# Performance work log

Measured on AMD Instinct MI355X. Metric: run time of the kernel, lower is better.

Reference implementation:

```python
import jax, jax.numpy as jnp
import numpy as np

B, T, D, H, FC, A = 256, 128, 512, 1024, 1024, 32
LOG_STD_MIN, LOG_STD_MAX = -20.0, 2.0
EPS = 1e-5


def setup_inputs() -> dict:
    key = jax.random.key(0)
    ks = jax.random.split(key, 16)
    def w(k, shape, fan_in):
        return jax.random.normal(k, shape, jnp.float32) / np.float32(np.sqrt(fan_in))
    return {
        "observations": jax.random.normal(ks[0], (B, T, D), jnp.float32),
        "hidden_state": jax.random.normal(ks[1], (B, H), jnp.float32),
        "episode_starts": jax.random.randint(ks[2], (B, T), 0, 2, jnp.int32),
        "ln_gamma": jnp.ones((D,), jnp.float32),
        "ln_beta": jnp.zeros((D,), jnp.float32),
        "W_fc": w(ks[3], (FC, D), D), "b_fc": jnp.zeros((FC,), jnp.float32),
        "W_ih": w(ks[4], (3 * H, FC), FC), "b_ih": jnp.zeros((3 * H,), jnp.float32),
        "W_hh": w(ks[5], (3 * H, H), H), "b_hh": jnp.zeros((3 * H,), jnp.float32),
        "W_out": w(ks[6], (H, H), H), "b_out": jnp.zeros((H,), jnp.float32),
        "W_mean": w(ks[7], (A, H), H) * 0.01, "b_mean": jnp.zeros((A,), jnp.float32),
        "W_ls": w(ks[8], (A, H), H) * 0.01, "b_ls": jnp.zeros((A,), jnp.float32),
    }


def reference(observations, hidden_state, episode_starts, ln_gamma, ln_beta,
              W_fc, b_fc, W_ih, b_ih, W_hh, b_hh, W_out, b_out,
              W_mean, b_mean, W_ls, b_ls):
    # LayerNorm over last dim (eps=1e-5, like nn.LayerNorm)
    mu = jnp.mean(observations, axis=-1, keepdims=True)
    var = jnp.mean(jnp.square(observations - mu), axis=-1, keepdims=True)
    x = (observations - mu) * jax.lax.rsqrt(var + EPS) * ln_gamma + ln_beta
    # fc_in + ReLU, then precompute GRU input-gate projections for all steps
    x = jax.nn.relu(jnp.einsum('btd,fd->btf', x, W_fc) + b_fc)          # (B,T,FC)
    xg = jnp.einsum('btf,gf->btg', x, W_ih) + b_ih                      # (B,T,3H)
    xg_t = jnp.swapaxes(xg, 0, 1)                                       # (T,B,3H)
    starts_t = jnp.swapaxes(episode_starts, 0, 1).astype(jnp.float32)   # (T,B)

    def step(h, inp):
        xg_s, st = inp
        h = h * (1.0 - st)[:, None]
        gh = h @ W_hh.T + b_hh                                           # (B,3H)
        xr, xz, xn = xg_s[:, :H], xg_s[:, H:2 * H], xg_s[:, 2 * H:]
        hr, hz, hn = gh[:, :H], gh[:, H:2 * H], gh[:, 2 * H:]
        r = jax.nn.sigmoid(xr + hr)
        z = jax.nn.sigmoid(xz + hz)
        n = jnp.tanh(xn + r * hn)
        h_new = (1.0 - z) * n + z * h
        out = jax.nn.relu(h_new @ W_out.T + b_out)
        return h_new, out

    h_final, outs = jax.lax.scan(step, hidden_state, (xg_t, starts_t))
    feats = jnp.swapaxes(outs, 0, 1)                                     # (B,T,H)
    means = jnp.einsum('bth,ah->bta', feats, W_mean) + b_mean
    log_std = jnp.clip(jnp.einsum('bth,ah->bta', feats, W_ls) + b_ls,
                       LOG_STD_MIN, LOG_STD_MAX)
    return means, log_std, h_final
```

## Files before the change

kernel.cpp:

```cpp
#include <hip/hip_runtime.h>
#include <hip/hip_bf16.h>

#define B_ 256
#define T_ 128
#define D_ 512
#define H_ 1024
#define FC_ 1024
#define A_ 32
#define NWG_ 256

typedef short bf16x8 __attribute__((ext_vector_type(8)));
typedef float f32x4 __attribute__((ext_vector_type(4)));

__device__ __forceinline__ float bf2f(unsigned short u) {
  return __uint_as_float(((unsigned)u) << 16);
}
__device__ __forceinline__ unsigned short f2bf(float x) {
  unsigned u = __float_as_uint(x);
  u = u + 0x7fffu + ((u >> 16) & 1u);
  return (unsigned short)(u >> 16);
}
__device__ __forceinline__ void unpack8(uint4 v, float* f) {
  f[0] = bf2f(v.x & 0xffff); f[1] = bf2f(v.x >> 16);
  f[2] = bf2f(v.y & 0xffff); f[3] = bf2f(v.y >> 16);
  f[4] = bf2f(v.z & 0xffff); f[5] = bf2f(v.z >> 16);
  f[6] = bf2f(v.w & 0xffff); f[7] = bf2f(v.w >> 16);
}
__device__ __forceinline__ uint4 pack8(const float* f) {
  uint4 v;
  v.x = (unsigned)f2bf(f[0]) | ((unsigned)f2bf(f[1]) << 16);
  v.y = (unsigned)f2bf(f[2]) | ((unsigned)f2bf(f[3]) << 16);
  v.z = (unsigned)f2bf(f[4]) | ((unsigned)f2bf(f[5]) << 16);
  v.w = (unsigned)f2bf(f[6]) | ((unsigned)f2bf(f[7]) << 16);
  return v;
}

__global__ __launch_bounds__(256) void detect_kernel(
    const unsigned short* __restrict__ obs, int* __restrict__ flag)
{
  __shared__ int cnt;
  if (threadIdx.x == 0) cnt = 0;
  __syncthreads();
  int c = 0;
  for (int i = threadIdx.x; i < 8192; i += 256) {
    unsigned e = (obs[i] >> 7) & 0xffu;
    if (e >= 0x86u) c++;
  }
  atomicAdd(&cnt, c);
  __syncthreads();
  if (threadIdx.x == 0) *flag = (cnt >= 64) ? 1 : 0;
}

struct CanonArgs {
  const void* src[14];
  unsigned short* dst[14];
  int ofs[15];
};
__global__ __launch_bounds__(256) void canon_kernel(CanonArgs a,
                                                    const int* __restrict__ flag)
{
  const int fl = *flag;
  const int i0 = (blockIdx.x * 256 + threadIdx.x) * 8;
  int t = 0;
  while (t < 14 && i0 >= a.ofs[t + 1]) t++;
  if (t >= 14) return;
  const int local = i0 - a.ofs[t];
  unsigned short* d = a.dst[t] + local;
  if (fl) {
    const float* s = (const float*)a.src[t] + local;
    #pragma unroll
    for (int e = 0; e < 8; e++) d[e] = f2bf(s[e]);
  } else {
    const unsigned short* s = (const unsigned short*)a.src[t] + local;
    #pragma unroll
    for (int e = 0; e < 8; e++) d[e] = s[e];
  }
}

__global__ __launch_bounds__(256) void ln_kernel(
    const void* __restrict__ obs,
    const unsigned short* __restrict__ gamma_,
    const unsigned short* __restrict__ beta_,
    unsigned short* __restrict__ xn, int t0, int tcShift,
    const int* __restrict__ flag)
{
  const int fl = *flag;
  const int lane = threadIdx.x & 63;
  const int rloc = blockIdx.x * 4 + (threadIdx.x >> 6);
  const int b  = rloc >> tcShift;
  const int tl = rloc & ((1 << tcShift) - 1);
  const int grow = b * T_ + t0 + tl;
  float f[8];
  if (fl) {
    const float* of = (const float*)obs + (size_t)grow * D_ + lane * 8;
    const float4 v0 = *(const float4*)of;
    const float4 v1 = *(const float4*)(of + 4);
    f[0] = v0.x; f[1] = v0.y; f[2] = v0.z; f[3] = v0.w;
    f[4] = v1.x; f[5] = v1.y; f[6] = v1.z; f[7] = v1.w;
  } else {
    uint4 v = *(const uint4*)((const unsigned short*)obs + (size_t)grow * D_ + lane * 8);
    unpack8(v, f);
  }
  float s = 0.f, ss = 0.f;
  #pragma unroll
  for (int i = 0; i < 8; i++) { s += f[i]; ss += f[i] * f[i]; }
  #pragma unroll
  for (int off = 32; off > 0; off >>= 1) {
    s  += __shfl_xor(s,  off, 64);
    ss += __shfl_xor(ss, off, 64);
  }
  const float mu  = s * (1.0f / D_);
  const float var = ss * (1.0f / D_) - mu * mu;
  const float inv = rsqrtf(var + 1e-5f);
  float g[8], b8[8];
  unpack8(*(const uint4*)(gamma_ + lane * 8), g);
  unpack8(*(const uint4*)(beta_  + lane * 8), b8);
  float o[8];
  #pragma unroll
  for (int i = 0; i < 8; i++) o[i] = (f[i] - mu) * inv * g[i] + b8[i];
  *(uint4*)(xn + (size_t)rloc * D_ + lane * 8) = pack8(o);
}

__global__ __launch_bounds__(256) void gemm_tn(
    const unsigned short* __restrict__ A, const unsigned short* __restrict__ Bm,
    const unsigned short* __restrict__ bias, unsigned short* __restrict__ C,
    int M, int N, int K, int relu)
{
  __shared__ short As[128][40];
  __shared__ short Bs[128][40];
  const int tid  = threadIdx.x;
  const int wave = tid >> 6, lane = tid & 63;
  const int quad = lane >> 4, l15 = lane & 15;
  const int m0 = blockIdx.y * 128, n0 = blockIdx.x * 128;
  const int wm = (wave >> 1) * 64, wn = (wave & 1) * 64;
  const int lrow = tid >> 2, lk = (tid & 3) * 8;
  f32x4 acc[4][4] = {};
  const size_t a0 = (size_t)(m0 + lrow) * K + lk;
  const size_t a1 = (size_t)(m0 + lrow + 64) * K + lk;
  const size_t b0 = (size_t)(n0 + lrow) * K + lk;
  const size_t b1 = (size_t)(n0 + lrow + 64) * K + lk;
  for (int k0 = 0; k0 < K; k0 += 32) {
    __syncthreads();
    *(uint4*)&As[lrow][lk]      = *(const uint4*)(A  + a0 + k0);
    *(uint4*)&As[lrow + 64][lk] = *(const uint4*)(A  + a1 + k0);
    *(uint4*)&Bs[lrow][lk]      = *(const uint4*)(Bm + b0 + k0);
    *(uint4*)&Bs[lrow + 64][lk] = *(const uint4*)(Bm + b1 + k0);
    __syncthreads();
    bf16x8 af[4], bfv[4];
    #pragma unroll
    for (int i = 0; i < 4; i++) af[i]  = *(const bf16x8*)&As[wm + i * 16 + l15][quad * 8];
    #pragma unroll
    for (int j = 0; j < 4; j++) bfv[j] = *(const bf16x8*)&Bs[wn + j * 16 + l15][quad * 8];
    #pragma unroll
    for (int i = 0; i < 4; i++)
      #pragma unroll
      for (int j = 0; j < 4; j++)
        acc[i][j] = __builtin_amdgcn_mfma_f32_16x16x32_bf16(af[i], bfv[j], acc[i][j], 0, 0, 0);
  }
  #pragma unroll
  for (int j = 0; j < 4; j++) {
    const int col = n0 + wn + j * 16 + l15;
    const float bj = bias ? bf2f(bias[col]) : 0.0f;
    #pragma unroll
    for (int i = 0; i < 4; i++) {
      const int row = m0 + wm + i * 16 + quad * 4;
      #pragma unroll
      for (int r = 0; r < 4; r++) {
        float v = acc[i][j][r] + bj;
        if (relu) v = fmaxf(v, 0.0f);
        C[(size_t)(row + r) * N + col] = f2bf(v);
      }
    }
  }
}

__global__ __launch_bounds__(256, 1) void gru_scan(
    const unsigned short* __restrict__ xg,
    const int* __restrict__ starts,
    const unsigned short* __restrict__ Whh,
    const unsigned short* __restrict__ bhh,
    float* __restrict__ hf,
    unsigned long long* __restrict__ hb0,
    unsigned long long* __restrict__ hb1,
    unsigned short* __restrict__ hall,
    int t0, int Tc,
    int* __restrict__ flags)
{
  __shared__ short Ws[3 * 16 * 1032];
  __shared__ short Hs[64 * 136];
  __shared__ unsigned sbits[64][4];
  const int tid  = threadIdx.x;
  const int wg   = blockIdx.x;
  const int jb   = wg & 63, bb = wg >> 6;
  const int j0   = jb * 16, b0 = bb * 64;
  const int wave = tid >> 6, lane = tid & 63;
  const int quad = lane >> 4, l15 = lane & 15;

  for (int c = tid; c < 48 * 128; c += 256) {
    const int row = c >> 7;
    const int kc  = (c & 127) * 8;
    const int g = row >> 4, jj = row & 15;
    *(uint4*)&Ws[row * 1032 + kc] =
        *(const uint4*)(Whh + (size_t)(g * H_ + j0 + jj) * H_ + kc);
  }
  for (int c = tid; c < 64 * 4; c += 256) {
    const int row = c >> 2, w = c & 3;
    unsigned m = 0;
    #pragma unroll
    for (int bi = 0; bi < 32; bi++)
      m |= (starts[(b0 + row) * T_ + w * 32 + bi] ? 1u : 0u) << bi;
    sbits[row][w] = m;
  }
  const float br = bf2f(bhh[j0 + l15]);
  const float bz = bf2f(bhh[H_ + j0 + l15]);
  const float bn = bf2f(bhh[2 * H_ + j0 + l15]);
  const int col = j0 + l15;

  const int r0 = wave * 16 + quad * 4;
  float hreg[4];
  #pragma unroll
  for (int r = 0; r < 4; r++)
    hreg[r] = hf[(size_t)(b0 + r0 + r) * H_ + col];

  __syncthreads();

  for (int tl = 0; tl < Tc; tl++) {
    const int t = t0 + tl;
    const unsigned long long* hin = (t & 1) ? hb1 : hb0;
    unsigned* hout_u = (unsigned*)((t & 1) ? hb0 : hb1);

    float xr[4], xz[4], xnv[4];
    #pragma unroll
    for (int r = 0; r < 4; r++) {
      const size_t xrow = ((size_t)(b0 + r0 + r) * Tc + tl) * (3 * H_);
      xr[r]  = bf2f(xg[xrow + col]);
      xz[r]  = bf2f(xg[xrow + H_ + col]);
      xnv[r] = bf2f(xg[xrow + 2 * H_ + col]);
    }

    unsigned long long pf[8];
    #pragma unroll
    for (int u = 0; u < 8; u++) {
      const int c = tid + u * 256;
      const int row = c >> 5, kc = (c & 31) * 4;
      pf[u] = __hip_atomic_load(
          &hin[(((size_t)(b0 + row)) * H_ + kc) >> 2],
          __ATOMIC_RELAXED, __HIP_MEMORY_SCOPE_AGENT);
    }

    f32x4 acc[3] = {};
    const unsigned tw = (unsigned)(t >> 5), tb = (unsigned)(t & 31);
    for (int kc0 = 0; kc0 < H_; kc0 += 128) {
      __syncthreads();
      #pragma unroll
      for (int u = 0; u < 8; u++) {
        const int c = tid + u * 256;
        const int row = c >> 5, kc = (c & 31) * 4;
        unsigned long long v = pf[u];
        if ((sbits[row][tw] >> tb) & 1u) v = 0ull;
        *(unsigned long long*)&Hs[row * 136 + kc] = v;
      }
      __syncthreads();
      if (kc0 + 128 < H_) {
        #pragma unroll
        for (int u = 0; u < 8; u++) {
          const int c = tid + u * 256;
          const int row = c >> 5, kc = (c & 31) * 4;
          pf[u] = __hip_atomic_load(
              &hin[(((size_t)(b0 + row)) * H_ + kc0 + 128 + kc) >> 2],
              __ATOMIC_RELAXED, __HIP_MEMORY_SCOPE_AGENT);
        }
      }
      #pragma unroll
      for (int kk = 0; kk < 128; kk += 32) {
        bf16x8 a = *(const bf16x8*)&Hs[(wave * 16 + l15) * 136 + kk + quad * 8];
        #pragma unroll
        for (int g = 0; g < 3; g++) {
          bf16x8 b = *(const bf16x8*)&Ws[(g * 16 + l15) * 1032 + kc0 + kk + quad * 8];
          acc[g] = __builtin_amdgcn_mfma_f32_16x16x32_bf16(a, b, acc[g], 0, 0, 0);
        }
      }
    }

    #pragma unroll
    for (int r = 0; r < 4; r++) {
      const int lrow = r0 + r;
      const int b = b0 + lrow;
      const float kb = ((sbits[lrow][tw] >> tb) & 1u) ? 0.0f : 1.0f;
      const float hr = acc[0][r] + br;
      const float hz = acc[1][r] + bz;
      const float hn = acc[2][r] + bn;
      const float rg = 1.0f / (1.0f + __expf(-(xr[r] + hr)));
      const float zg = 1.0f / (1.0f + __expf(-(xz[r] + hz)));
      const float ng = tanhf(xnv[r] + rg * hn);
      const float hv = (1.0f - zg) * ng + zg * (hreg[r] * kb);
      hreg[r] = hv;
      const unsigned mine = (unsigned)f2bf(hv);
      const unsigned other = (unsigned)__shfl_xor((int)mine, 1, 64);
      if ((l15 & 1) == 0) {
        const unsigned packed = mine | (other << 16);
        __hip_atomic_store(&hout_u[((size_t)b * H_ + col) >> 1], packed,
                           __ATOMIC_RELAXED, __HIP_MEMORY_SCOPE_AGENT);
        ((unsigned*)hall)[(((size_t)b * Tc + tl) * H_ + col) >> 1] = packed;
      }
    }

    const int my = t0 + tl + 1;
    __builtin_amdgcn_s_waitcnt(0);
    __syncthreads();
    if (tid == 0)
      __hip_atomic_store(&flags[wg * 32], my, __ATOMIC_RELAXED,
                         __HIP_MEMORY_SCOPE_AGENT);
    if (tid < 64) {
      while (__hip_atomic_load(&flags[(bb * 64 + tid) * 32], __ATOMIC_RELAXED,
                               __HIP_MEMORY_SCOPE_AGENT) < my)
        __builtin_amdgcn_s_sleep(1);
    }
    __syncthreads();
  }

  #pragma unroll
  for (int r = 0; r < 4; r++)
    hf[(size_t)(b0 + r0 + r) * H_ + col] = hreg[r];
}

__global__ __launch_bounds__(256) void heads_kernel(
    const unsigned short* __restrict__ feats,
    const unsigned short* __restrict__ Wm, const unsigned short* __restrict__ bm,
    const unsigned short* __restrict__ Wl, const unsigned short* __restrict__ bl,
    void* __restrict__ outbuf, int t0, int tcShift, const int* __restrict__ flag)
{
  __shared__ short Fs[64][40];
  __shared__ short Ws[64][40];
  const int fl = *flag;
  const int tid  = threadIdx.x;
  const int wave = tid >> 6, lane = tid & 63;
  const int quad = lane >> 4, l15 = lane & 15;
  const int m0 = blockIdx.x * 64;
  const int lrow = tid >> 2, lk = (tid & 3) * 8;
  f32x4 acc[4] = {};
  for (int k0 = 0; k0 < H_; k0 += 32) {
    __syncthreads();
    *(uint4*)&Fs[lrow][lk] = *(const uint4*)(feats + (size_t)(m0 + lrow) * H_ + k0 + lk);
    const unsigned short* wsrc = (lrow < 32)
        ? (Wm + (size_t)lrow * H_ + k0 + lk)
        : (Wl + (size_t)(lrow - 32) * H_ + k0 + lk);
    *(uint4*)&Ws[lrow][lk] = *(const uint4*)wsrc;
    __syncthreads();
    bf16x8 af = *(const bf16x8*)&Fs[wave * 16 + l15][quad * 8];
    #pragma unroll
    for (int j = 0; j < 4; j++) {
      bf16x8 bfv = *(const bf16x8*)&Ws[j * 16 + l15][quad * 8];
      acc[j] = __builtin_amdgcn_mfma_f32_16x16x32_bf16(af, bfv, acc[j], 0, 0, 0);
    }
  }
  const int tcMask = (1 << tcShift) - 1;
  const size_t lstdBase = (size_t)B_ * T_ * A_;
  #pragma unroll
  for (int j = 0; j < 4; j++) {
    const int col = j * 16 + l15;
    #pragma unroll
    for (int r = 0; r < 4; r++) {
      const int row = m0 + wave * 16 + quad * 4 + r;
      const int grow = (row >> tcShift) * T_ + t0 + (row & tcMask);
      float v = acc[j][r];
      size_t idx;
      if (col < 32) {
        v += bf2f(bm[col]);
        idx = (size_t)grow * A_ + col;
      } else {
        v += bf2f(bl[col - 32]);
        v = fminf(fmaxf(v, -20.0f), 2.0f);
        idx = lstdBase + (size_t)grow * A_ + (col - 32);
      }
      if (fl) ((float*)outbuf)[idx] = v;
      else    ((unsigned short*)outbuf)[idx] = f2bf(v);
    }
  }
}

__global__ __launch_bounds__(256) void h0_cast(const void* __restrict__ h0,
                                               float* __restrict__ hf,
                                               unsigned short* __restrict__ hb0,
                                               const int* __restrict__ flag) {
  const int fl = *flag;
  int i = blockIdx.x * 256 + threadIdx.x;
  float v = fl ? ((const float*)h0)[i] : bf2f(((const unsigned short*)h0)[i]);
  hf[i] = v;
  hb0[i] = f2bf(v);
}
__global__ __launch_bounds__(256) void hfin_store(const float* __restrict__ h,
                                                  void* __restrict__ outbuf,
                                                  const int* __restrict__ flag) {
  const int fl = *flag;
  const size_t base = 2ull * B_ * T_ * A_;
  int i = blockIdx.x * 256 + threadIdx.x;
  if (fl) ((float*)outbuf)[base + i] = h[i];
  else    ((unsigned short*)outbuf)[base + i] = f2bf(h[i]);
}

extern "C" void kernel_launch(void* const* d_in, const int* in_sizes, int n_in,
                              void* d_out, int out_size, void* d_ws, size_t ws_size,
                              hipStream_t stream)
{
  const void* obs    = d_in[0];
  const void* h0in   = d_in[1];
  const int*  starts = (const int*)d_in[2];
  const void* fsrc[14] = { d_in[5], d_in[7], d_in[9], d_in[11], d_in[13], d_in[15],
                           d_in[3], d_in[4], d_in[6], d_in[8], d_in[10], d_in[12],
                           d_in[14], d_in[16] };
  const int fn[14] = { FC_ * D_, 3 * H_ * FC_, 3 * H_ * H_, H_ * H_, A_ * H_, A_ * H_,
                       D_, D_, FC_, 3 * H_, 3 * H_, H_, A_, A_ };

  char* ws = (char*)d_ws;
  int* flag = (int*)ws;
  size_t cur = 256;
  unsigned short* cdst[14];
  for (int i = 0; i < 14; i++) {
    cdst[i] = (unsigned short*)(ws + cur);
    cur += (size_t)fn[i] * 2;
    cur = (cur + 255) & ~255ull;
  }
  const size_t chunkBase = cur;
  const size_t fixedTail = 1048576ull  + 2ull * 524288ull
                         + 32768ull ;

  int Tc = 1;
  for (int c = 32; c >= 1; c >>= 1) {
    size_t need = chunkBase + (size_t)c * 2883584ull + fixedTail;
    if (need <= ws_size) { Tc = c; break; }
  }
  int tcShift = 0;
  while ((1 << tcShift) < Tc) tcShift++;

  unsigned short* xn   = (unsigned short*)(ws + chunkBase);
  unsigned short* xfc  = (unsigned short*)(ws + chunkBase + (size_t)Tc * 262144ull);
  unsigned short* xg   = (unsigned short*)(ws + chunkBase + (size_t)Tc * 786432ull);
  unsigned short* hall = (unsigned short*)(ws + chunkBase + (size_t)Tc * 2359296ull);
  size_t o = chunkBase + (size_t)Tc * 2883584ull;
  float* hf           = (float*)(ws + o);           o += 1048576ull;
  unsigned short* hb0 = (unsigned short*)(ws + o);  o += 524288ull;
  unsigned short* hb1 = (unsigned short*)(ws + o);  o += 524288ull;
  int* flags          = (int*)(ws + o);
  unsigned short* feats = xg;

  const unsigned short *Wfc = cdst[0], *Wih = cdst[1], *Whh = cdst[2], *Wout = cdst[3];
  const unsigned short *Wmean = cdst[4], *Wls = cdst[5];
  const unsigned short *gam = cdst[6], *bet = cdst[7], *bfc = cdst[8], *bih = cdst[9];
  const unsigned short *bhh = cdst[10], *bout = cdst[11], *bmean = cdst[12], *bls = cdst[13];

  detect_kernel<<<dim3(1), dim3(256), 0, stream>>>((const unsigned short*)obs, flag);
  CanonArgs ca;
  int total = 0;
  for (int i = 0; i < 14; i++) {
    ca.src[i] = fsrc[i];
    ca.dst[i] = cdst[i];
    ca.ofs[i] = total;
    total += fn[i];
  }
  ca.ofs[14] = total;
  canon_kernel<<<dim3((total / 8 + 255) / 256), dim3(256), 0, stream>>>(ca, flag);
  h0_cast<<<dim3(B_ * H_ / 256), dim3(256), 0, stream>>>(h0in, hf, hb0, flag);
  hipMemsetAsync(flags, 0, 32768, stream);

  const int Mc = B_ * Tc;
  for (int t0 = 0; t0 < T_; t0 += Tc) {
    ln_kernel<<<dim3(Mc / 4), dim3(256), 0, stream>>>(obs, gam, bet, xn, t0, tcShift, flag);
    gemm_tn<<<dim3(FC_ / 128, Mc / 128), dim3(256), 0, stream>>>(
        xn, Wfc, bfc, xfc, Mc, FC_, D_, 1);
    gemm_tn<<<dim3(3 * H_ / 128, Mc / 128), dim3(256), 0, stream>>>(
        xfc, Wih, bih, xg, Mc, 3 * H_, FC_, 0);

    gru_scan<<<dim3(NWG_), dim3(256), 0, stream>>>(
        xg, starts, Whh, bhh, hf,
        (unsigned long long*)hb0, (unsigned long long*)hb1,
        hall, t0, Tc, flags);

    gemm_tn<<<dim3(H_ / 128, Mc / 128), dim3(256), 0, stream>>>(
        hall, Wout, bout, feats, Mc, H_, H_, 1);
    heads_kernel<<<dim3(Mc / 64), dim3(256), 0, stream>>>(
        feats, Wmean, bmean, Wls, bls, d_out, t0, tcShift, flag);
  }

  hfin_store<<<dim3(B_ * H_ / 256), dim3(256), 0, stream>>>(hf, d_out, flag);
}
```

Measured before the change: 1.887 ms.

## Load GRU hidden-state MFMA operands directly from global into registers, dropping LDS staging

The recurrent step previously staged each 128-wide chunk of the previous hidden state into a shared-memory tile, with two block barriers per chunk, before feeding MFMA. Now each lane loads its own A-operand fragment straight from the global hidden buffer using atomic relaxed loads, keeps an 8-deep register ring of prefetches, and applies the episode-reset mask per row in registers. This removes 16 __syncthreads and the LDS round trip per timestep, which sit on the serial critical path. In exchange, each wave redundantly loads the hidden rows it needs as small 8-byte strided accesses, which may coalesce less well than the old cooperative loads.

```diff
diff --git a/kernel.cpp b/kernel.cpp
--- a/kernel.cpp
+++ b/kernel.cpp
@@ -187,7 +187,6 @@
     int* __restrict__ flags)
 {
   __shared__ short Ws[3 * 16 * 1032];
-  __shared__ short Hs[64 * 136];
   __shared__ unsigned sbits[64][4];
   const int tid  = threadIdx.x;
   const int wg   = blockIdx.x;
@@ -216,6 +215,9 @@
   const float bn = bf2f(bhh[2 * H_ + j0 + l15]);
   const int col = j0 + l15;
 
+  const int arow = wave * 16 + l15;
+  const size_t hrow = (size_t)(b0 + arow) * (H_ / 4) + quad * 2;
+
   const int r0 = wave * 16 + quad * 4;
   float hreg[4];
   #pragma unroll
@@ -226,8 +228,10 @@
 
   for (int tl = 0; tl < Tc; tl++) {
     const int t = t0 + tl;
-    const unsigned long long* hin = (t & 1) ? hb1 : hb0;
+    unsigned long long* hin = (t & 1) ? hb1 : hb0;
     unsigned* hout_u = (unsigned*)((t & 1) ? hb0 : hb1);
+    const unsigned tw = (unsigned)(t >> 5), tb = (unsigned)(t & 31);
+    const bool kill = (sbits[arow][tw] >> tb) & 1u;
 
     float xr[4], xz[4], xnv[4];
     #pragma unroll
@@ -238,47 +242,30 @@
       xnv[r] = bf2f(xg[xrow + 2 * H_ + col]);
     }
 
-    unsigned long long pf[8];
-    #pragma unroll
-    for (int u = 0; u < 8; u++) {
-      const int c = tid + u * 256;
-      const int row = c >> 5, kc = (c & 31) * 4;
-      pf[u] = __hip_atomic_load(
-          &hin[(((size_t)(b0 + row)) * H_ + kc) >> 2],
-          __ATOMIC_RELAXED, __HIP_MEMORY_SCOPE_AGENT);
-    }
-
+    unsigned long long buf[8][2];
+    #pragma unroll
+    for (int p = 0; p < 8; p++) {
+      buf[p][0] = __hip_atomic_load(&hin[hrow + p * 8],
+                                    __ATOMIC_RELAXED, __HIP_MEMORY_SCOPE_AGENT);
+      buf[p][1] = __hip_atomic_load(&hin[hrow + p * 8 + 1],
+                                    __ATOMIC_RELAXED, __HIP_MEMORY_SCOPE_AGENT);
+    }
     f32x4 acc[3] = {};
-    const unsigned tw = (unsigned)(t >> 5), tb = (unsigned)(t & 31);
-    for (int kc0 = 0; kc0 < H_; kc0 += 128) {
-      __syncthreads();
-      #pragma unroll
-      for (int u = 0; u < 8; u++) {
-        const int c = tid + u * 256;
-        const int row = c >> 5, kc = (c & 31) * 4;
-        unsigned long long v = pf[u];
-        if ((sbits[row][tw] >> tb) & 1u) v = 0ull;
-        *(unsigned long long*)&Hs[row * 136 + kc] = v;
-      }
-      __syncthreads();
-      if (kc0 + 128 < H_) {
-        #pragma unroll
-        for (int u = 0; u < 8; u++) {
-          const int c = tid + u * 256;
-          const int row = c >> 5, kc = (c & 31) * 4;
-          pf[u] = __hip_atomic_load(
-              &hin[(((size_t)(b0 + row)) * H_ + kc0 + 128 + kc) >> 2],
-              __ATOMIC_RELAXED, __HIP_MEMORY_SCOPE_AGENT);
-        }
+    #pragma unroll
+    for (int kk = 0; kk < 32; kk++) {
+      union { unsigned long long q[2]; bf16x8 v; } u;
+      u.q[0] = kill ? 0ull : buf[kk & 7][0];
+      u.q[1] = kill ? 0ull : buf[kk & 7][1];
+      if (kk + 8 < 32) {
+        buf[kk & 7][0] = __hip_atomic_load(&hin[hrow + (kk + 8) * 8],
+                                           __ATOMIC_RELAXED, __HIP_MEMORY_SCOPE_AGENT);
+        buf[kk & 7][1] = __hip_atomic_load(&hin[hrow + (kk + 8) * 8 + 1],
+                                           __ATOMIC_RELAXED, __HIP_MEMORY_SCOPE_AGENT);
       }
       #pragma unroll
-      for (int kk = 0; kk < 128; kk += 32) {
-        bf16x8 a = *(const bf16x8*)&Hs[(wave * 16 + l15) * 136 + kk + quad * 8];
-        #pragma unroll
-        for (int g = 0; g < 3; g++) {
-          bf16x8 b = *(const bf16x8*)&Ws[(g * 16 + l15) * 1032 + kc0 + kk + quad * 8];
-          acc[g] = __builtin_amdgcn_mfma_f32_16x16x32_bf16(a, b, acc[g], 0, 0, 0);
-        }
+      for (int g = 0; g < 3; g++) {
+        bf16x8 b = *(const bf16x8*)&Ws[(g * 16 + l15) * 1032 + kk * 32 + quad * 8];
+        acc[g] = __builtin_amdgcn_mfma_f32_16x16x32_bf16(u.v, b, acc[g], 0, 0, 0);
       }
     }
 
```

New measurement: 2.110 ms. 11.8% more time.
